# Kernel optimization log

Measured on AMD Instinct MI355X. Metric: run time of the kernel, lower is better.

The kernel has to match this reference:

```python
import jax, jax.numpy as jnp
import numpy as np

B, T1, H, P, V = 4096, 65, 64, 50, 32
D = H + P  # input_size = 114


def setup_inputs() -> dict:
    key = jax.random.key(0)
    ks = jax.random.split(key, 20)
    s = 1.0 / np.sqrt(D)
    sh = 1.0 / np.sqrt(H)
    inp = {
        "phonetic_input": jax.random.normal(ks[0], (B, P), dtype=jnp.float32),
        "char_seq": jax.random.randint(ks[1], (B, T1), 0, V, dtype=jnp.int64),
        "emb": jax.random.normal(ks[2], (V, H), dtype=jnp.float32).at[0].set(0.0),  # padding_idx=0
        "W_rx": jax.random.uniform(ks[3], (D, H), jnp.float32, -s, s),
        "b_rx": jax.random.uniform(ks[4], (H,), jnp.float32, -s, s),
        "W_rh": jax.random.uniform(ks[5], (H, H), jnp.float32, -sh, sh),
        "b_rh": jax.random.uniform(ks[6], (H,), jnp.float32, -sh, sh),
        "W_zx": jax.random.uniform(ks[7], (D, H), jnp.float32, -s, s),
        "b_zx": jax.random.uniform(ks[8], (H,), jnp.float32, -s, s),
        "W_zh": jax.random.uniform(ks[9], (H, H), jnp.float32, -sh, sh),
        "b_zh": jax.random.uniform(ks[10], (H,), jnp.float32, -sh, sh),
        "W_hx": jax.random.uniform(ks[11], (D, H), jnp.float32, -s, s),
        "b_hx": jax.random.uniform(ks[12], (H,), jnp.float32, -s, s),
        "W_hh": jax.random.uniform(ks[13], (H, H), jnp.float32, -sh, sh),
        "b_hh": jax.random.uniform(ks[14], (H,), jnp.float32, -sh, sh),
        "W_proj": jax.random.uniform(ks[15], (H, V), jnp.float32, -sh, sh),
        "b_proj": jax.random.uniform(ks[16], (V,), jnp.float32, -sh, sh),
    }
    return inp


def reference(phonetic_input, char_seq, emb, W_rx, b_rx, W_rh, b_rh, W_zx, b_zx,
              W_zh, b_zh, W_hx, b_hx, W_hh, b_hh, W_proj, b_proj):
    input_seq = char_seq[:, :-1]          # [B, T]
    target_seq = char_seq[:, 1:]          # [B, T]
    Bsz, T = input_seq.shape

    char_emb = emb[input_seq]                                   # [B, T, H]
    phon = jnp.broadcast_to(phonetic_input[:, None, :], (Bsz, T, P))
    x = jnp.concatenate([char_emb, phon], axis=2)               # [B, T, D]

    # Hoist input-side projections into batched GEMMs, [T, B, H] for scan
    xr = jnp.einsum('btd,dh->tbh', x, W_rx) + b_rx
    xz = jnp.einsum('btd,dh->tbh', x, W_zx) + b_zx
    xh = jnp.einsum('btd,dh->tbh', x, W_hx) + b_hx

    h0 = jnp.zeros((Bsz, H), dtype=x.dtype)

    def step(h, inputs):
        xr_t, xz_t, xh_t = inputs
        r = jax.nn.sigmoid(xr_t + h @ W_rh + b_rh)
        z = jax.nn.sigmoid(xz_t + h @ W_zh + b_zh)
        c = jnp.tanh(xh_t + (r * h) @ W_hh + b_hh)
        h_new = (1.0 - z) * h + z * c
        return h_new, h_new

    _, hs = jax.lax.scan(step, h0, (xr, xz, xh))                # [T, B, H]
    logits = jnp.einsum('tbh,hv->btv', hs, W_proj) + b_proj     # [B, T, V]

    # cross_entropy with ignore_index=0 (mean over non-ignored)
    targets = target_seq.reshape(-1)
    logp = jax.nn.log_softmax(logits.reshape(-1, V), axis=-1)
    nll = -jnp.take_along_axis(logp, targets[:, None], axis=-1)[:, 0]
    mask = (targets != 0).astype(logits.dtype)
    loss = jnp.sum(nll * mask) / jnp.maximum(jnp.sum(mask), 1.0)
    return logits, loss
```

## Files before the change

kernel.cpp:

```cpp
#include <hip/hip_runtime.h>
#include <stdint.h>

#define Bsz 4096
#define Tn  64
#define T1n 65
#define Hn  64
#define Pn  50
#define Vn  32

typedef __attribute__((ext_vector_type(8))) short short8;
typedef __attribute__((ext_vector_type(4))) float floatx4;

__device__ __forceinline__ float bf2f(unsigned short u) {
  union { unsigned int i; float f; } x; x.i = ((unsigned int)u) << 16; return x.f;
}
__device__ __forceinline__ unsigned short f2bf(float f) {
  union { float f; unsigned int i; } x; x.f = f;
  return (unsigned short)((x.i + 0x7FFFu + ((x.i >> 16) & 1u)) >> 16);
}
__device__ __forceinline__ float fast_sigmoid(float x) {
  return __builtin_amdgcn_rcpf(1.f + __expf(-x));
}
__device__ __forceinline__ float fast_tanh(float x) {
  return 1.f - 2.f * __builtin_amdgcn_rcpf(1.f + __expf(2.f * x));
}

__device__ __forceinline__ short8 load_bfrag(const float* __restrict__ W, int ncols, int col, int kbase) {
  short8 f;
#pragma unroll
  for (int j = 0; j < 8; ++j) f[j] = (short)f2bf(W[(long)(kbase + j) * ncols + col]);
  return f;
}

__launch_bounds__(512)
__global__ void gru_kernel(const float* __restrict__ phon,
                           const int* __restrict__ cs,
                           const float* __restrict__ emb,
                           const float* __restrict__ Wrx, const float* __restrict__ brx,
                           const float* __restrict__ Wrh, const float* __restrict__ brh,
                           const float* __restrict__ Wzx, const float* __restrict__ bzx,
                           const float* __restrict__ Wzh, const float* __restrict__ bzh,
                           const float* __restrict__ Whx, const float* __restrict__ bhx,
                           const float* __restrict__ Whh, const float* __restrict__ bhh,
                           const float* __restrict__ Wpj, const float* __restrict__ bpj_g,
                           float* __restrict__ ws,
                           float* __restrict__ outp) {
  __shared__ unsigned short tbl_s[3 * 32 * 66];
  __shared__ __align__(16) unsigned short hist_s[8 * 1152];
  __shared__ __align__(16) unsigned short rh_s[1152];
  __shared__ float z_s[16 * 68];
  __shared__ float logit_s[8 * 16 * 33];
  __shared__ unsigned int code4_s[(T1n + 1) * 4];
  __shared__ int det_s[1];
  __shared__ float red_s[16];

  const int tid = threadIdx.x;
  const int b0 = blockIdx.x * 16;
  const int W8 = tid >> 6, lane = tid & 63, q = lane >> 4, c16 = lane & 15;
  const bool isScan = (W8 < 4);
  const int w = isScan ? W8 : (W8 - 4);
  const int jcol = w * 16 + c16;
  const floatx4 zf = {0.f, 0.f, 0.f, 0.f};

  if (tid == 0) det_s[0] = 0;
  __syncthreads();
  if (tid < 128 && cs[2 * tid + 1] != 0) atomicOr(&det_s[0], 1);
  __syncthreads();
  const bool is64 = (det_s[0] == 0);

  for (int i = tid; i < 1152; i += 512) hist_s[7 * 1152 + i] = 0;
  for (int i = tid; i < T1n * 4; i += 512) {
    int t = i >> 2, qq = i & 3;
    unsigned int pk = 0;
#pragma unroll
    for (int r = 0; r < 4; ++r) {
      long idx = (long)(b0 + qq * 4 + r) * T1n + t;
      int c = is64 ? cs[2 * idx] : cs[idx];
      pk |= ((unsigned int)(c & 255)) << (8 * r);
    }
    code4_s[i] = pk;
  }

  for (int g = 0; g < 3; ++g) {
    const float* Wg = (g == 0) ? Wrx : (g == 1) ? Wzx : Whx;
    const float* bx = (g == 0) ? brx : (g == 1) ? bzx : bhx;
    const float* bh = (g == 0) ? brh : (g == 1) ? bzh : bhh;
    float acc[4] = {0.f, 0.f, 0.f, 0.f};
    float bias = bx[lane] + bh[lane];
    for (int d = 0; d < Hn; ++d) {
      float wv = Wg[(long)d * Hn + lane];
#pragma unroll
      for (int k = 0; k < 4; ++k)
        acc[k] += emb[(long)(W8 + 8 * k) * Hn + d] * wv;
    }
#pragma unroll
    for (int k = 0; k < 4; ++k)
      tbl_s[g * 2112 + (W8 + 8 * k) * 66 + lane] = f2bf(acc[k] + bias);
  }

  float ph_a[4] = {0.f, 0.f, 0.f, 0.f};
  float ph_h[4] = {0.f, 0.f, 0.f, 0.f};
  {
    const float* Wa = isScan ? Wrx : Wzx;
    for (int p = 0; p < Pn; ++p) {
      float wa = Wa[(long)(Hn + p) * Hn + jcol];
      float wh = isScan ? Whx[(long)(Hn + p) * Hn + jcol] : 0.f;
#pragma unroll
      for (int r = 0; r < 4; ++r) {
        float xv = phon[(long)(b0 + q * 4 + r) * Pn + p];
        ph_a[r] += xv * wa;
        ph_h[r] += xv * wh;
      }
    }
  }

  short8 Ba0, Ba1;
  short8 Bh0, Bh1;
  short8 Bp0, Bp1;
  float bpj = 0.f;
  {
    const float* Wa = isScan ? Wrh : Wzh;
    Ba0 = load_bfrag(Wa, Hn, jcol, q * 8);
    Ba1 = load_bfrag(Wa, Hn, jcol, 32 + q * 8);
    Bh0 = Ba0; Bh1 = Ba1; Bp0 = Ba0; Bp1 = Ba1;
    if (isScan) {
      Bh0 = load_bfrag(Whh, Hn, jcol, q * 8);
      Bh1 = load_bfrag(Whh, Hn, jcol, 32 + q * 8);
    } else if (W8 < 6) {
      int vt = W8 - 4;
      Bp0 = load_bfrag(Wpj, Vn, vt * 16 + c16, q * 8);
      Bp1 = load_bfrag(Wpj, Vn, vt * 16 + c16, 32 + q * 8);
      bpj = bpj_g[vt * 16 + c16];
    }
  }

  float h[4] = {0.f, 0.f, 0.f, 0.f};
  float nll = 0.f, cnt = 0.f;

  __syncthreads();

  for (int t = 0; t < Tn; ++t) {
    const unsigned int pk = code4_s[t * 4 + q];
    {
      const unsigned short* hp = &hist_s[((t + 7) & 7) * 1152];
      short8 a0 = *(const short8*)&hp[c16 * 72 + q * 8];
      short8 a1 = *(const short8*)&hp[c16 * 72 + 32 + q * 8];
      floatx4 acc = __builtin_amdgcn_mfma_f32_16x16x32_bf16(a0, Ba0, zf, 0, 0, 0);
      acc = __builtin_amdgcn_mfma_f32_16x16x32_bf16(a1, Ba1, acc, 0, 0, 0);
      if (isScan) {
#pragma unroll
        for (int r = 0; r < 4; ++r) {
          int cr = (pk >> (8 * r)) & 255;
          float xr = bf2f(tbl_s[0 * 2112 + cr * 66 + jcol]) + ph_a[r] + acc[r];
          rh_s[(q * 4 + r) * 72 + jcol] = f2bf(fast_sigmoid(xr) * h[r]);
        }
      } else {
#pragma unroll
        for (int r = 0; r < 4; ++r) {
          int cr = (pk >> (8 * r)) & 255;
          float xz = bf2f(tbl_s[1 * 2112 + cr * 66 + jcol]) + ph_a[r] + acc[r];
          z_s[(q * 4 + r) * 68 + jcol] = fast_sigmoid(xz);
        }
      }
    }
    __syncthreads();

    if (isScan) {
      short8 p0 = *(const short8*)&rh_s[c16 * 72 + q * 8];
      short8 p1 = *(const short8*)&rh_s[c16 * 72 + 32 + q * 8];
      floatx4 acc = __builtin_amdgcn_mfma_f32_16x16x32_bf16(p0, Bh0, zf, 0, 0, 0);
      acc = __builtin_amdgcn_mfma_f32_16x16x32_bf16(p1, Bh1, acc, 0, 0, 0);
      unsigned short* hw = &hist_s[(t & 7) * 1152];
#pragma unroll
      for (int r = 0; r < 4; ++r) {
        int cr = (pk >> (8 * r)) & 255;
        float xh = bf2f(tbl_s[2 * 2112 + cr * 66 + jcol]) + ph_h[r] + acc[r];
        float c = fast_tanh(xh);
        float zr = z_s[(q * 4 + r) * 68 + jcol];
        float hn = (1.f - zr) * h[r] + zr * c;
        h[r] = hn;
        hw[(q * 4 + r) * 72 + jcol] = f2bf(hn);
      }
    } else if (W8 < 6 && t > 0) {
      const unsigned short* hp = &hist_s[((t + 7) & 7) * 1152];
      short8 a0 = *(const short8*)&hp[c16 * 72 + q * 8];
      short8 a1 = *(const short8*)&hp[c16 * 72 + 32 + q * 8];
      floatx4 l = __builtin_amdgcn_mfma_f32_16x16x32_bf16(a0, Bp0, zf, 0, 0, 0);
      l = __builtin_amdgcn_mfma_f32_16x16x32_bf16(a1, Bp1, l, 0, 0, 0);
      float* pg = &logit_s[((t - 1) & 7) * 528];
      int vt = W8 - 4;
#pragma unroll
      for (int r = 0; r < 4; ++r)
        pg[(q * 4 + r) * 33 + vt * 16 + c16] = l[r] + bpj;
    }
    __syncthreads();

    if ((t & 7) == 7) {
      int p = t - 8 + W8;
      if (p >= 0) {
        const float* pg = &logit_s[(p & 7) * 528];
        int v = lane & 31, hf = lane >> 5;
        unsigned int pk1 = 0;
#pragma unroll
        for (int i = 0; i < 8; ++i) {
          int m = i * 2 + hf;
          float lg = pg[m * 33 + v];
          float s = __expf(lg);
#pragma unroll
          for (int off = 16; off >= 1; off >>= 1) s += __shfl_xor(s, off);
          float lse = __logf(s);
          outp[(((long)(b0 + m)) * Tn + p) * Vn + v] = lg;
          pk1 = code4_s[(p + 1) * 4 + (m >> 2)];
          int targ = (pk1 >> (8 * (m & 3))) & 255;
          if (targ != 0 && v == targ) { nll += lse - lg; cnt += 1.f; }
        }
      }
    }
  }

  __syncthreads();
  if (W8 >= 4 && W8 < 6) {
    const unsigned short* hp = &hist_s[7 * 1152];
    short8 a0 = *(const short8*)&hp[c16 * 72 + q * 8];
    short8 a1 = *(const short8*)&hp[c16 * 72 + 32 + q * 8];
    floatx4 l = __builtin_amdgcn_mfma_f32_16x16x32_bf16(a0, Bp0, zf, 0, 0, 0);
    l = __builtin_amdgcn_mfma_f32_16x16x32_bf16(a1, Bp1, l, 0, 0, 0);
    int vt = W8 - 4;
#pragma unroll
    for (int r = 0; r < 4; ++r)
      logit_s[7 * 528 + (q * 4 + r) * 33 + vt * 16 + c16] = l[r] + bpj;
  }
  __syncthreads();
  if (W8 == 0) {
    const float* pg = &logit_s[7 * 528];
    int v = lane & 31, hf = lane >> 5;
#pragma unroll
    for (int i = 0; i < 8; ++i) {
      int m = i * 2 + hf;
      float lg = pg[m * 33 + v];
      float s = __expf(lg);
#pragma unroll
      for (int off = 16; off >= 1; off >>= 1) s += __shfl_xor(s, off);
      float lse = __logf(s);
      outp[(((long)(b0 + m)) * Tn + 63) * Vn + v] = lg;
      unsigned int pk1 = code4_s[64 * 4 + (m >> 2)];
      int targ = (pk1 >> (8 * (m & 3))) & 255;
      if (targ != 0 && v == targ) { nll += lse - lg; cnt += 1.f; }
    }
  }

#pragma unroll
  for (int off = 32; off >= 1; off >>= 1) {
    nll += __shfl_xor(nll, off);
    cnt += __shfl_xor(cnt, off);
  }
  if (lane == 0) { red_s[W8] = nll; red_s[8 + W8] = cnt; }
  __syncthreads();
  if (tid == 0) {
    float n = 0.f, c = 0.f;
#pragma unroll
    for (int i = 0; i < 8; ++i) { n += red_s[i]; c += red_s[8 + i]; }
    ws[2 * blockIdx.x] = n;
    ws[2 * blockIdx.x + 1] = c;
  }
}

__global__ void loss_kernel(const float* __restrict__ ws, float* __restrict__ outp) {
  int lane = threadIdx.x;
  float n = 0.f, c = 0.f;
  for (int i = lane; i < Bsz / 16; i += 64) { n += ws[2 * i]; c += ws[2 * i + 1]; }
#pragma unroll
  for (int off = 32; off >= 1; off >>= 1) {
    n += __shfl_xor(n, off);
    c += __shfl_xor(c, off);
  }
  if (lane == 0) outp[(size_t)Bsz * Tn * Vn] = n / fmaxf(c, 1.f);
}

extern "C" void kernel_launch(void* const* d_in, const int* in_sizes, int n_in,
                              void* d_out, int out_size, void* d_ws, size_t ws_size,
                              hipStream_t stream) {
  const float* phon = (const float*)d_in[0];
  const int*   cs   = (const int*)d_in[1];
  const float* emb  = (const float*)d_in[2];
  const float* Wrx  = (const float*)d_in[3];
  const float* brx  = (const float*)d_in[4];
  const float* Wrh  = (const float*)d_in[5];
  const float* brh  = (const float*)d_in[6];
  const float* Wzx  = (const float*)d_in[7];
  const float* bzx  = (const float*)d_in[8];
  const float* Wzh  = (const float*)d_in[9];
  const float* bzh  = (const float*)d_in[10];
  const float* Whx  = (const float*)d_in[11];
  const float* bhx  = (const float*)d_in[12];
  const float* Whh  = (const float*)d_in[13];
  const float* bhh  = (const float*)d_in[14];
  const float* Wpj  = (const float*)d_in[15];
  const float* bpj  = (const float*)d_in[16];
  float* ws = (float*)d_ws;

  hipLaunchKernelGGL(gru_kernel, dim3(Bsz / 16), dim3(512), 0, stream,
                     phon, cs, emb, Wrx, brx, Wrh, brh, Wzx, bzx, Wzh, bzh,
                     Whx, bhx, Whh, bhh, Wpj, bpj, ws, (float*)d_out);
  hipLaunchKernelGGL(loss_kernel, dim3(1), dim3(64), 0, stream, ws, (float*)d_out);
}
```

Measured before the change: 175.1 us.

## Transpose MFMA operands so each lane owns 4 contiguous columns for vector LDS access

Swaps the A/B operands of every MFMA so the output fragment gives each lane one batch row and four consecutive hidden columns. The gate-table lookups, z_s, rh_s, hist_s and logit_s accesses can then use 4-wide vector loads and stores in place of scalar strided ones. The char-code storage becomes a per-row byte array read one word per four steps. Logit and z strides are padded for 16-byte alignment, which may change LDS bank-conflict patterns, and the phonetic projection now uses vector weight loads.

```diff
diff --git a/kernel.cpp b/kernel.cpp
--- a/kernel.cpp
+++ b/kernel.cpp
@@ -9,6 +9,7 @@
 #define Vn  32
 
 typedef __attribute__((ext_vector_type(8))) short short8;
+typedef __attribute__((ext_vector_type(4))) short short4v;
 typedef __attribute__((ext_vector_type(4))) float floatx4;
 
 __device__ __forceinline__ float bf2f(unsigned short u) {
@@ -45,12 +46,12 @@
                            const float* __restrict__ Wpj, const float* __restrict__ bpj_g,
                            float* __restrict__ ws,
                            float* __restrict__ outp) {
-  __shared__ unsigned short tbl_s[3 * 32 * 66];
+  __shared__ unsigned short tbl_s[3 * 2112];
   __shared__ __align__(16) unsigned short hist_s[8 * 1152];
   __shared__ __align__(16) unsigned short rh_s[1152];
-  __shared__ float z_s[16 * 68];
-  __shared__ float logit_s[8 * 16 * 33];
-  __shared__ unsigned int code4_s[(T1n + 1) * 4];
+  __shared__ __align__(16) float z_s[16 * 68];
+  __shared__ __align__(16) float logit_s[8 * 576];
+  __shared__ unsigned char code_s[16 * 68];
   __shared__ int det_s[1];
   __shared__ float red_s[16];
 
@@ -60,6 +61,7 @@
   const bool isScan = (W8 < 4);
   const int w = isScan ? W8 : (W8 - 4);
   const int jcol = w * 16 + c16;
+  const int jc4 = w * 16 + q * 4;
   const floatx4 zf = {0.f, 0.f, 0.f, 0.f};
 
   if (tid == 0) det_s[0] = 0;
@@ -69,16 +71,11 @@
   const bool is64 = (det_s[0] == 0);
 
   for (int i = tid; i < 1152; i += 512) hist_s[7 * 1152 + i] = 0;
-  for (int i = tid; i < T1n * 4; i += 512) {
-    int t = i >> 2, qq = i & 3;
-    unsigned int pk = 0;
-#pragma unroll
-    for (int r = 0; r < 4; ++r) {
-      long idx = (long)(b0 + qq * 4 + r) * T1n + t;
-      int c = is64 ? cs[2 * idx] : cs[idx];
-      pk |= ((unsigned int)(c & 255)) << (8 * r);
-    }
-    code4_s[i] = pk;
+  for (int i = tid; i < 16 * T1n; i += 512) {
+    int m = i / T1n, t = i - m * T1n;
+    long idx = (long)(b0 + m) * T1n + t;
+    int c = is64 ? cs[2 * idx] : cs[idx];
+    code_s[m * 68 + t] = (unsigned char)c;
   }
 
   for (int g = 0; g < 3; ++g) {
@@ -103,13 +100,14 @@
   {
     const float* Wa = isScan ? Wrx : Wzx;
     for (int p = 0; p < Pn; ++p) {
-      float wa = Wa[(long)(Hn + p) * Hn + jcol];
-      float wh = isScan ? Whx[(long)(Hn + p) * Hn + jcol] : 0.f;
-#pragma unroll
-      for (int r = 0; r < 4; ++r) {
-        float xv = phon[(long)(b0 + q * 4 + r) * Pn + p];
-        ph_a[r] += xv * wa;
-        ph_h[r] += xv * wh;
+      float xv = phon[(long)(b0 + c16) * Pn + p];
+      floatx4 wa4 = *(const floatx4*)&Wa[(long)(Hn + p) * Hn + jc4];
+#pragma unroll
+      for (int r = 0; r < 4; ++r) ph_a[r] += xv * wa4[r];
+      if (isScan) {
+        floatx4 wh4 = *(const floatx4*)&Whx[(long)(Hn + p) * Hn + jc4];
+#pragma unroll
+        for (int r = 0; r < 4; ++r) ph_h[r] += xv * wh4[r];
       }
     }
   }
@@ -117,7 +115,8 @@
   short8 Ba0, Ba1;
   short8 Bh0, Bh1;
   short8 Bp0, Bp1;
-  float bpj = 0.f;
+  floatx4 bpj4 = zf;
+  const int vt = W8 - 4;
   {
     const float* Wa = isScan ? Wrh : Wzh;
     Ba0 = load_bfrag(Wa, Hn, jcol, q * 8);
@@ -127,91 +126,90 @@
       Bh0 = load_bfrag(Whh, Hn, jcol, q * 8);
       Bh1 = load_bfrag(Whh, Hn, jcol, 32 + q * 8);
     } else if (W8 < 6) {
-      int vt = W8 - 4;
       Bp0 = load_bfrag(Wpj, Vn, vt * 16 + c16, q * 8);
       Bp1 = load_bfrag(Wpj, Vn, vt * 16 + c16, 32 + q * 8);
-      bpj = bpj_g[vt * 16 + c16];
+      bpj4 = *(const floatx4*)&bpj_g[vt * 16 + q * 4];
     }
   }
 
   float h[4] = {0.f, 0.f, 0.f, 0.f};
   float nll = 0.f, cnt = 0.f;
+  unsigned int cw = 0;
 
   __syncthreads();
 
   for (int t = 0; t < Tn; ++t) {
-    const unsigned int pk = code4_s[t * 4 + q];
-    {
-      const unsigned short* hp = &hist_s[((t + 7) & 7) * 1152];
-      short8 a0 = *(const short8*)&hp[c16 * 72 + q * 8];
-      short8 a1 = *(const short8*)&hp[c16 * 72 + 32 + q * 8];
-      floatx4 acc = __builtin_amdgcn_mfma_f32_16x16x32_bf16(a0, Ba0, zf, 0, 0, 0);
-      acc = __builtin_amdgcn_mfma_f32_16x16x32_bf16(a1, Ba1, acc, 0, 0, 0);
-      if (isScan) {
-#pragma unroll
-        for (int r = 0; r < 4; ++r) {
-          int cr = (pk >> (8 * r)) & 255;
-          float xr = bf2f(tbl_s[0 * 2112 + cr * 66 + jcol]) + ph_a[r] + acc[r];
-          rh_s[(q * 4 + r) * 72 + jcol] = f2bf(fast_sigmoid(xr) * h[r]);
-        }
-      } else {
-#pragma unroll
-        for (int r = 0; r < 4; ++r) {
-          int cr = (pk >> (8 * r)) & 255;
-          float xz = bf2f(tbl_s[1 * 2112 + cr * 66 + jcol]) + ph_a[r] + acc[r];
-          z_s[(q * 4 + r) * 68 + jcol] = fast_sigmoid(xz);
-        }
+    if ((t & 3) == 0) cw = *(const unsigned int*)&code_s[c16 * 68 + t];
+    const int crb = (cw >> ((t & 3) * 8)) & 255;
+
+    const unsigned short* hp = &hist_s[((t + 7) & 7) * 1152];
+    short8 hb0 = *(const short8*)&hp[c16 * 72 + q * 8];
+    short8 hb1 = *(const short8*)&hp[c16 * 72 + 32 + q * 8];
+    if (isScan) {
+      floatx4 acc = __builtin_amdgcn_mfma_f32_16x16x32_bf16(Ba0, hb0, zf, 0, 0, 0);
+      acc = __builtin_amdgcn_mfma_f32_16x16x32_bf16(Ba1, hb1, acc, 0, 0, 0);
+      short4v tr = *(const short4v*)&tbl_s[0 * 2112 + crb * 66 + jc4];
+      short4v rhp;
+#pragma unroll
+      for (int r = 0; r < 4; ++r) {
+        float xr = bf2f((unsigned short)tr[r]) + ph_a[r] + acc[r];
+        rhp[r] = (short)f2bf(fast_sigmoid(xr) * h[r]);
       }
+      *(short4v*)&rh_s[c16 * 72 + jc4] = rhp;
+    } else {
+      floatx4 acc = __builtin_amdgcn_mfma_f32_16x16x32_bf16(Ba0, hb0, zf, 0, 0, 0);
+      acc = __builtin_amdgcn_mfma_f32_16x16x32_bf16(Ba1, hb1, acc, 0, 0, 0);
+      short4v tz = *(const short4v*)&tbl_s[1 * 2112 + crb * 66 + jc4];
+      floatx4 z4;
+#pragma unroll
+      for (int r = 0; r < 4; ++r)
+        z4[r] = fast_sigmoid(bf2f((unsigned short)tz[r]) + ph_a[r] + acc[r]);
+      *(floatx4*)&z_s[c16 * 68 + jc4] = z4;
     }
     __syncthreads();
 
     if (isScan) {
       short8 p0 = *(const short8*)&rh_s[c16 * 72 + q * 8];
       short8 p1 = *(const short8*)&rh_s[c16 * 72 + 32 + q * 8];
-      floatx4 acc = __builtin_amdgcn_mfma_f32_16x16x32_bf16(p0, Bh0, zf, 0, 0, 0);
-      acc = __builtin_amdgcn_mfma_f32_16x16x32_bf16(p1, Bh1, acc, 0, 0, 0);
-      unsigned short* hw = &hist_s[(t & 7) * 1152];
+      floatx4 acc = __builtin_amdgcn_mfma_f32_16x16x32_bf16(Bh0, p0, zf, 0, 0, 0);
+      acc = __builtin_amdgcn_mfma_f32_16x16x32_bf16(Bh1, p1, acc, 0, 0, 0);
+      short4v th = *(const short4v*)&tbl_s[2 * 2112 + crb * 66 + jc4];
+      floatx4 z4 = *(const floatx4*)&z_s[c16 * 68 + jc4];
+      short4v hb4;
 #pragma unroll
       for (int r = 0; r < 4; ++r) {
-        int cr = (pk >> (8 * r)) & 255;
-        float xh = bf2f(tbl_s[2 * 2112 + cr * 66 + jcol]) + ph_h[r] + acc[r];
+        float xh = bf2f((unsigned short)th[r]) + ph_h[r] + acc[r];
         float c = fast_tanh(xh);
-        float zr = z_s[(q * 4 + r) * 68 + jcol];
-        float hn = (1.f - zr) * h[r] + zr * c;
+        float hn = (1.f - z4[r]) * h[r] + z4[r] * c;
         h[r] = hn;
-        hw[(q * 4 + r) * 72 + jcol] = f2bf(hn);
+        hb4[r] = (short)f2bf(hn);
       }
+      *(short4v*)&hist_s[(t & 7) * 1152 + c16 * 72 + jc4] = hb4;
     } else if (W8 < 6 && t > 0) {
-      const unsigned short* hp = &hist_s[((t + 7) & 7) * 1152];
-      short8 a0 = *(const short8*)&hp[c16 * 72 + q * 8];
-      short8 a1 = *(const short8*)&hp[c16 * 72 + 32 + q * 8];
-      floatx4 l = __builtin_amdgcn_mfma_f32_16x16x32_bf16(a0, Bp0, zf, 0, 0, 0);
-      l = __builtin_amdgcn_mfma_f32_16x16x32_bf16(a1, Bp1, l, 0, 0, 0);
-      float* pg = &logit_s[((t - 1) & 7) * 528];
-      int vt = W8 - 4;
-#pragma unroll
-      for (int r = 0; r < 4; ++r)
-        pg[(q * 4 + r) * 33 + vt * 16 + c16] = l[r] + bpj;
+      floatx4 l = __builtin_amdgcn_mfma_f32_16x16x32_bf16(Bp0, hb0, zf, 0, 0, 0);
+      l = __builtin_amdgcn_mfma_f32_16x16x32_bf16(Bp1, hb1, l, 0, 0, 0);
+      floatx4 lg4;
+#pragma unroll
+      for (int r = 0; r < 4; ++r) lg4[r] = l[r] + bpj4[r];
+      *(floatx4*)&logit_s[((t - 1) & 7) * 576 + c16 * 36 + vt * 16 + q * 4] = lg4;
     }
     __syncthreads();
 
     if ((t & 7) == 7) {
       int p = t - 8 + W8;
       if (p >= 0) {
-        const float* pg = &logit_s[(p & 7) * 528];
+        const float* pg = &logit_s[(p & 7) * 576];
         int v = lane & 31, hf = lane >> 5;
-        unsigned int pk1 = 0;
 #pragma unroll
         for (int i = 0; i < 8; ++i) {
           int m = i * 2 + hf;
-          float lg = pg[m * 33 + v];
+          float lg = pg[m * 36 + v];
           float s = __expf(lg);
 #pragma unroll
           for (int off = 16; off >= 1; off >>= 1) s += __shfl_xor(s, off);
           float lse = __logf(s);
           outp[(((long)(b0 + m)) * Tn + p) * Vn + v] = lg;
-          pk1 = code4_s[(p + 1) * 4 + (m >> 2)];
-          int targ = (pk1 >> (8 * (m & 3))) & 255;
+          int targ = code_s[m * 68 + p + 1];
           if (targ != 0 && v == targ) { nll += lse - lg; cnt += 1.f; }
         }
       }
@@ -223,28 +221,27 @@
     const unsigned short* hp = &hist_s[7 * 1152];
     short8 a0 = *(const short8*)&hp[c16 * 72 + q * 8];
     short8 a1 = *(const short8*)&hp[c16 * 72 + 32 + q * 8];
-    floatx4 l = __builtin_amdgcn_mfma_f32_16x16x32_bf16(a0, Bp0, zf, 0, 0, 0);
-    l = __builtin_amdgcn_mfma_f32_16x16x32_bf16(a1, Bp1, l, 0, 0, 0);
-    int vt = W8 - 4;
-#pragma unroll
-    for (int r = 0; r < 4; ++r)
-      logit_s[7 * 528 + (q * 4 + r) * 33 + vt * 16 + c16] = l[r] + bpj;
+    floatx4 l = __builtin_amdgcn_mfma_f32_16x16x32_bf16(Bp0, a0, zf, 0, 0, 0);
+    l = __builtin_amdgcn_mfma_f32_16x16x32_bf16(Bp1, a1, l, 0, 0, 0);
+    floatx4 lg4;
+#pragma unroll
+    for (int r = 0; r < 4; ++r) lg4[r] = l[r] + bpj4[r];
+    *(floatx4*)&logit_s[7 * 576 + c16 * 36 + vt * 16 + q * 4] = lg4;
   }
   __syncthreads();
   if (W8 == 0) {
-    const float* pg = &logit_s[7 * 528];
+    const float* pg = &logit_s[7 * 576];
     int v = lane & 31, hf = lane >> 5;
 #pragma unroll
     for (int i = 0; i < 8; ++i) {
       int m = i * 2 + hf;
-      float lg = pg[m * 33 + v];
+      float lg = pg[m * 36 + v];
       float s = __expf(lg);
 #pragma unroll
       for (int off = 16; off >= 1; off >>= 1) s += __shfl_xor(s, off);
       float lse = __logf(s);
       outp[(((long)(b0 + m)) * Tn + 63) * Vn + v] = lg;
-      unsigned int pk1 = code4_s[64 * 4 + (m >> 2)];
-      int targ = (pk1 >> (8 * (m & 3))) & 255;
+      int targ = code_s[m * 68 + 64];
       if (targ != 0 && v == targ) { nll += lse - lg; cnt += 1.f; }
     }
   }
```

Result: slower. 182.5 us (+4.3%).
